# Kernel optimization log

Measured on AMD Instinct MI355X. Metric: run time of the kernel, lower is better.

Reference implementation:

```python
import jax, jax.numpy as jnp
import numpy as np
import math

D_H = 256
H = 4
DK = 64  # d_h // num_heads

def _ff(x, w1, b1, w2, b2):
    # FeedForward: Linear -> GELU -> (dropout, eval=identity) -> Linear -> GELU
    h = jax.nn.gelu(x @ w1 + b1, approximate=False)
    return jax.nn.gelu(h @ w2 + b2, approximate=False)

def _attend(h_t, h_s, tgt, src, nw, num_t, m_w1, m_b1, m_w2, m_b2, Wq, Wk, Wv):
    E = tgt.shape[0]
    M_s = _ff(h_s, m_w1, m_b1, m_w2, m_b2)           # [N_s, d_h]
    Q = h_t @ Wq                                     # [N_t, H*DK]
    K = h_s @ Wk
    V = M_s @ Wv
    Qe = Q[tgt].reshape(E, H, DK)
    Ke = K[src].reshape(E, H, DK)
    Ve = V[src].reshape(E, H, DK)
    scores = (Qe * Ke).sum(-1) / math.sqrt(DK)       # [E, H]
    scores = scores + jnp.log(jnp.clip(nw, 1e-10))[:, None]
    # torch scatter_reduce amax with zeros init + include_self=True => max includes 0
    smax = jnp.maximum(jax.ops.segment_max(scores, tgt, num_segments=num_t), 0.0)
    ex = jnp.exp(scores - smax[tgt])
    sum_ex = jax.ops.segment_sum(ex, tgt, num_segments=num_t)
    attn = ex / (sum_ex[tgt] + 1e-10)                # [E, H]
    wV = (attn[:, :, None] * Ve).reshape(E, H * DK)
    return jax.ops.segment_sum(wV, tgt, num_segments=num_t)  # [N_t, d_h]

def setup_inputs() -> dict:
    key = jax.random.key(0)
    ks = jax.random.split(key, 20)
    I, A, E = 50000, 10000, 200000
    s = 0.05
    return {
        "inv_h": jax.random.normal(ks[0], (I, D_H), jnp.float32),
        "asset_h": jax.random.normal(ks[1], (A, D_H), jnp.float32),
        "inv_norm_w": jax.random.uniform(ks[2], (E,), jnp.float32),
        "asset_norm_w": jax.random.uniform(ks[3], (E,), jnp.float32),
        "m_w1": jax.random.normal(ks[4], (D_H, D_H), jnp.float32) * s,
        "m_b1": jnp.zeros((D_H,), jnp.float32),
        "m_w2": jax.random.normal(ks[5], (D_H, D_H), jnp.float32) * s,
        "m_b2": jnp.zeros((D_H,), jnp.float32),
        "Wq": jax.random.normal(ks[6], (D_H, H * DK), jnp.float32) * s,
        "Wk": jax.random.normal(ks[7], (D_H, H * DK), jnp.float32) * s,
        "Wv": jax.random.normal(ks[8], (D_H, H * DK), jnp.float32) * s,
        "u_w1": jax.random.normal(ks[9], (2 * D_H, D_H), jnp.float32) * s,
        "u_b1": jnp.zeros((D_H,), jnp.float32),
        "u_w2": jax.random.normal(ks[10], (D_H, D_H), jnp.float32) * s,
        "u_b2": jnp.zeros((D_H,), jnp.float32),
        "edge_tgt": jax.random.randint(ks[11], (E,), 0, I),
        "edge_src": jax.random.randint(ks[12], (E,), 0, A),
    }

def reference(inv_h, asset_h, inv_norm_w, asset_norm_w,
              m_w1, m_b1, m_w2, m_b2, Wq, Wk, Wv,
              u_w1, u_b1, u_w2, u_b2, edge_tgt, edge_src):
    I = inv_h.shape[0]
    A = asset_h.shape[0]
    # investors aggregate from assets: edge_index_ia = (inv, asset)
    inv_msg = _attend(inv_h, asset_h, edge_tgt, edge_src, inv_norm_w, I,
                      m_w1, m_b1, m_w2, m_b2, Wq, Wk, Wv)
    # assets aggregate from investors: reversed edges
    asset_msg = _attend(asset_h, inv_h, edge_src, edge_tgt, asset_norm_w, A,
                        m_w1, m_b1, m_w2, m_b2, Wq, Wk, Wv)
    inv_h_new = _ff(jnp.concatenate([inv_h, inv_msg], axis=-1), u_w1, u_b1, u_w2, u_b2)
    asset_h_new = _ff(jnp.concatenate([asset_h, asset_msg], axis=-1), u_w1, u_b1, u_w2, u_b2)
    return (inv_h_new, asset_h_new)
```

## Files before the change

### kernel.cpp

```cpp
#include <hip/hip_runtime.h>

typedef __bf16 bf16x8 __attribute__((ext_vector_type(8)));
typedef float f32x16 __attribute__((ext_vector_type(16)));
typedef unsigned short ushort8 __attribute__((ext_vector_type(8)));

__device__ __forceinline__ float gelu_exact(float x) {
    return 0.5f * x * (1.0f + erff(x * 0.70710678118654752440f));
}

__device__ __forceinline__ void gload_lds16(const void* g, void* l) {
    __builtin_amdgcn_global_load_lds(
        (const __attribute__((address_space(1))) unsigned int*)g,
        (__attribute__((address_space(3))) unsigned int*)l, 16, 0, 0);
}


__global__ __launch_bounds__(256) void count_kernel(
    const int* __restrict__ tgt, const int* __restrict__ src,
    int* __restrict__ cnt_i, int* __restrict__ cnt_a, int E)
{
    int e = blockIdx.x * 256 + threadIdx.x;
    if (e < E) {
        atomicAdd(&cnt_i[tgt[e]], 1);
        atomicAdd(&cnt_a[src[e]], 1);
    }
}

__global__ __launch_bounds__(256) void scan_block(
    const int* __restrict__ cnt, int* __restrict__ offs, int* __restrict__ bsum, int N)
{
    __shared__ int s[256];
    int i = blockIdx.x * 256 + threadIdx.x;
    int v = (i < N) ? cnt[i] : 0;
    s[threadIdx.x] = v;
    __syncthreads();
    for (int d = 1; d < 256; d <<= 1) {
        int t = (threadIdx.x >= d) ? s[threadIdx.x - d] : 0;
        __syncthreads();
        s[threadIdx.x] += t;
        __syncthreads();
    }
    if (i < N) offs[i] = s[threadIdx.x] - v;
    if (threadIdx.x == 255) bsum[blockIdx.x] = s[255];
}

__global__ __launch_bounds__(256) void scan_bsum(int* __restrict__ bsum, int nb)
{
    __shared__ int s[256];
    int v = (threadIdx.x < nb) ? bsum[threadIdx.x] : 0;
    s[threadIdx.x] = v;
    __syncthreads();
    for (int d = 1; d < 256; d <<= 1) {
        int t = (threadIdx.x >= d) ? s[threadIdx.x - d] : 0;
        __syncthreads();
        s[threadIdx.x] += t;
        __syncthreads();
    }
    if (threadIdx.x < nb) bsum[threadIdx.x] = s[threadIdx.x] - v;
}

__global__ __launch_bounds__(256) void add_offs(
    int* __restrict__ offs, int* __restrict__ cursor,
    const int* __restrict__ bsum, int N, int E)
{
    int i = blockIdx.x * 256 + threadIdx.x;
    if (i < N) {
        int f = offs[i] + bsum[blockIdx.x];
        offs[i] = f;
        cursor[i] = f;
    }
    if (i == 0) offs[N] = E;
}

__global__ __launch_bounds__(256) void fill_kernel(
    const int* __restrict__ tgt, const int* __restrict__ src,
    const float* __restrict__ nw_i, const float* __restrict__ nw_a,
    int* __restrict__ cur_i, int* __restrict__ cur_a,
    int* __restrict__ src_i, float* __restrict__ lw_i,
    int* __restrict__ src_a, float* __restrict__ lw_a, int E)
{
    int e = blockIdx.x * 256 + threadIdx.x;
    if (e < E) {
        int t = tgt[e], s = src[e];
        float li = logf(fmaxf(nw_i[e], 1e-10f));
        float la = logf(fmaxf(nw_a[e], 1e-10f));
        int p = atomicAdd(&cur_i[t], 1);
        src_i[p] = s; lw_i[p] = li;
        int q = atomicAdd(&cur_a[s], 1);
        src_a[q] = t; lw_a[q] = la;
    }
}

struct PrepArgs {
    const float* src[7];
    unsigned short* hi[7];
    unsigned short* lo[7];
    int K[7];
    int off[8];
};

__global__ __launch_bounds__(256) void prep_w(PrepArgs a)
{
    int s = blockIdx.x * 256 + threadIdx.x;
    if (s >= a.off[7]) return;
    int m = 0;
    #pragma unroll
    for (int i = 0; i < 6; ++i) m += (s >= a.off[i + 1]) ? 1 : 0;
    int sl = s - a.off[m];
    int KB = a.K[m] >> 4;
    int l  = sl & 63;
    int kb = (sl >> 6) % KB;
    int nb = (sl >> 6) / KB;
    int n  = nb * 32 + (l & 31);
    int k0 = kb * 16 + ((l >> 5) << 3);
    ushort8 hh, ll;
    #pragma unroll
    for (int i = 0; i < 8; ++i) {
        float x = a.src[m][(size_t)(k0 + i) * 256 + n];
        __bf16 h = (__bf16)x;
        hh[i] = __builtin_bit_cast(unsigned short, h);
        ll[i] = __builtin_bit_cast(unsigned short, (__bf16)(x - (float)h));
    }
    *(ushort8*)(a.hi[m] + (size_t)sl * 8) = hh;
    *(ushort8*)(a.lo[m] + (size_t)sl * 8) = ll;
}

__global__ __launch_bounds__(256) void pack_rows(
    const float* __restrict__ X, unsigned short* __restrict__ Ph,
    unsigned short* __restrict__ Pl, int M, int RB)
{
    int s = blockIdx.x * 256 + threadIdx.x;
    int total = RB * 16 * 64;
    if (s >= total) return;
    int l  = s & 63;
    int kb = (s >> 6) & 15;
    int rb = s >> 10;
    int row = min(rb * 32 + (l & 31), M - 1);
    int k0  = kb * 16 + ((l >> 5) << 3);
    const float* p = X + (size_t)row * 256 + k0;
    float4 f0 = *(const float4*)p;
    float4 f1 = *(const float4*)(p + 4);
    float xs[8] = {f0.x, f0.y, f0.z, f0.w, f1.x, f1.y, f1.z, f1.w};
    ushort8 hh, ll;
    #pragma unroll
    for (int i = 0; i < 8; ++i) {
        __bf16 h = (__bf16)xs[i];
        hh[i] = __builtin_bit_cast(unsigned short, h);
        ll[i] = __builtin_bit_cast(unsigned short, (__bf16)(xs[i] - (float)h));
    }
    *(ushort8*)(Ph + (size_t)s * 8) = hh;
    *(ushort8*)(Pl + (size_t)s * 8) = ll;
}

__global__ __launch_bounds__(256) void fused_attn(
    const float* __restrict__ Q, const float* __restrict__ Kk, const float* __restrict__ V,
    const int* __restrict__ offs, const int* __restrict__ srcs,
    const float* __restrict__ lws,
    float* __restrict__ scbuf, unsigned short* __restrict__ msgH,
    unsigned short* __restrict__ msgL, int T)
{
    int w = blockIdx.x * 4 + (threadIdx.x >> 6);
    int lane = threadIdx.x & 63;
    if (w >= T) return;
    int t = w;
    int beg = offs[t], end = offs[t + 1];
    int h = lane >> 4;

    float4 q = *(const float4*)(Q + (size_t)t * 256 + lane * 4);

    float mx = 0.f;
    {
        int sN = 0; float lC = 0.f, lN = 0.f;
        float4 k0 = make_float4(0.f, 0.f, 0.f, 0.f);
        if (beg < end) {
            int s0 = srcs[beg];
            lC = lws[beg];
            k0 = *(const float4*)(Kk + (size_t)s0 * 256 + lane * 4);
        }
        if (beg + 1 < end) { sN = srcs[beg + 1]; lN = lws[beg + 1]; }
        for (int j = beg; j < end; ++j) {
            int sNN = 0; float lNN = 0.f;
            if (j + 2 < end) { sNN = srcs[j + 2]; lNN = lws[j + 2]; }
            float4 k1 = k0;
            if (j + 1 < end) k1 = *(const float4*)(Kk + (size_t)sN * 256 + lane * 4);
            float d = q.x * k0.x + q.y * k0.y + q.z * k0.z + q.w * k0.w;
            d += __shfl_xor(d, 1);
            d += __shfl_xor(d, 2);
            d += __shfl_xor(d, 4);
            d += __shfl_xor(d, 8);
            float sc = d * 0.125f + lC;
            if ((lane & 15) == 0) scbuf[(size_t)j * 4 + h] = sc;
            mx = fmaxf(mx, sc);
            k0 = k1; lC = lN; sN = sNN; lN = lNN;
        }
    }

    float sum = 0.f;
    float4 macc = make_float4(0.f, 0.f, 0.f, 0.f);
    {
        int sN = 0; float scC = 0.f, scN = 0.f;
        float4 v0 = make_float4(0.f, 0.f, 0.f, 0.f);
        if (beg < end) {
            int s0 = srcs[beg];
            scC = scbuf[(size_t)beg * 4 + h];
            v0 = *(const float4*)(V + (size_t)s0 * 256 + lane * 4);
        }
        if (beg + 1 < end) { sN = srcs[beg + 1]; scN = scbuf[(size_t)(beg + 1) * 4 + h]; }
        for (int j = beg; j < end; ++j) {
            int sNN = 0; float scNN = 0.f;
            if (j + 2 < end) { sNN = srcs[j + 2]; scNN = scbuf[(size_t)(j + 2) * 4 + h]; }
            float4 v1 = v0;
            if (j + 1 < end) v1 = *(const float4*)(V + (size_t)sN * 256 + lane * 4);
            float ex = expf(scC - mx);
            sum += ex;
            macc.x += ex * v0.x; macc.y += ex * v0.y;
            macc.z += ex * v0.z; macc.w += ex * v0.w;
            v0 = v1; scC = scN; sN = sNN; scN = scNN;
        }
    }
    float inv = 1.f / (sum + 1e-10f);
    float vals[4] = {macc.x * inv, macc.y * inv, macc.z * inv, macc.w * inv};
    unsigned short hs[4], ls[4];
    #pragma unroll
    for (int i = 0; i < 4; ++i) {
        __bf16 hh = (__bf16)vals[i];
        hs[i] = __builtin_bit_cast(unsigned short, hh);
        ls[i] = __builtin_bit_cast(unsigned short, (__bf16)(vals[i] - (float)hh));
    }
    size_t base = (((size_t)(t >> 5) * 16 + (lane >> 2)) * 64 + ((lane >> 1) & 1) * 32 + (t & 31)) * 8
                + ((lane & 1) << 2);
    *(ushort4*)(msgH + base) = make_ushort4(hs[0], hs[1], hs[2], hs[3]);
    *(ushort4*)(msgL + base) = make_ushort4(ls[0], ls[1], ls[2], ls[3]);
}

template<int CONCAT, int PACKOUT>
__global__ __launch_bounds__(256, 2) void gemm_pk(
    const unsigned short* __restrict__ Ah, const unsigned short* __restrict__ Al,
    const unsigned short* __restrict__ A2h, const unsigned short* __restrict__ A2l,
    const unsigned short* __restrict__ Bh, const unsigned short* __restrict__ Bl,
    const float* __restrict__ bias, int act, int M,
    float* __restrict__ Cf, unsigned short* __restrict__ Ch, unsigned short* __restrict__ Cl)
{
    const int KB = CONCAT ? 32 : 16;
    const int NS = CONCAT ? 8 : 4;
    const int RB = (M + 31) >> 5;
    const int lane = threadIdx.x & 63;
    const int w = threadIdx.x >> 6;
    const int rbb = blockIdx.x * 2;
    const int nb0 = w * 2;

    __shared__ union {
        unsigned short stage[3][2][2][4][512];
        float tbuf[4][32 * 33];
    } sm __attribute__((aligned(16)));

    f32x16 acc[2][2] = {};

    auto stage_one = [&](int bufn, int st, int u) {
        int half = u >> 3, rb = (u >> 2) & 1, kb = u & 3;
        int kbg = st * 4 + kb;
        const unsigned short* srcp;
        int kba = kbg;
        if (CONCAT && kbg >= 16) { kba = kbg - 16; srcp = half ? A2l : A2h; }
        else                     { srcp = half ? Al : Ah; }
        int rbl = min(rbb + rb, RB - 1);
        const unsigned short* g = srcp + ((size_t)(rbl * 16 + kba) * 64 + lane) * 8;
        gload_lds16(g, &sm.stage[bufn][half][rb][kb][0]);
    };

    #pragma unroll
    for (int i = 0; i < 4; ++i) stage_one(0, 0, w * 4 + i);
    #pragma unroll
    for (int i = 0; i < 4; ++i) stage_one(1, 1, w * 4 + i);
    asm volatile("s_waitcnt vmcnt(4)" ::: "memory");
    __builtin_amdgcn_s_barrier();

    for (int st = 0; st < NS; ++st) {
        if (st) {
            asm volatile("s_waitcnt vmcnt(20)" ::: "memory");
            __builtin_amdgcn_s_barrier();
        }
        const int buf = st % 3;

        ushort8 Breg[4][4];
        #pragma unroll
        for (int kb = 0; kb < 4; ++kb) {
            int kbg = st * 4 + kb;
            size_t t0 = ((size_t)((nb0 + 0) * KB + kbg) * 64 + lane) * 8;
            size_t t1 = ((size_t)((nb0 + 1) * KB + kbg) * 64 + lane) * 8;
            Breg[kb][0] = *(const ushort8*)(Bh + t0);
            Breg[kb][1] = *(const ushort8*)(Bl + t0);
            Breg[kb][2] = *(const ushort8*)(Bh + t1);
            Breg[kb][3] = *(const ushort8*)(Bl + t1);
        }

        {
            int bufn = (st + 2) % 3;
            int stc = (st + 2 < NS) ? (st + 2) : (NS - 1);
            #pragma unroll
            for (int i = 0; i < 4; ++i) stage_one(bufn, stc, w * 4 + i);
        }

        #pragma unroll
        for (int kb = 0; kb < 4; ++kb) {
            bf16x8 a0h = __builtin_bit_cast(bf16x8, *(const ushort8*)&sm.stage[buf][0][0][kb][lane * 8]);
            bf16x8 a0l = __builtin_bit_cast(bf16x8, *(const ushort8*)&sm.stage[buf][1][0][kb][lane * 8]);
            bf16x8 a1h = __builtin_bit_cast(bf16x8, *(const ushort8*)&sm.stage[buf][0][1][kb][lane * 8]);
            bf16x8 a1l = __builtin_bit_cast(bf16x8, *(const ushort8*)&sm.stage[buf][1][1][kb][lane * 8]);
            bf16x8 b0h = __builtin_bit_cast(bf16x8, Breg[kb][0]);
            bf16x8 b0l = __builtin_bit_cast(bf16x8, Breg[kb][1]);
            bf16x8 b1h = __builtin_bit_cast(bf16x8, Breg[kb][2]);
            bf16x8 b1l = __builtin_bit_cast(bf16x8, Breg[kb][3]);
            acc[0][0] = __builtin_amdgcn_mfma_f32_32x32x16_bf16(a0h, b0h, acc[0][0], 0, 0, 0);
            acc[0][0] = __builtin_amdgcn_mfma_f32_32x32x16_bf16(a0h, b0l, acc[0][0], 0, 0, 0);
            acc[0][0] = __builtin_amdgcn_mfma_f32_32x32x16_bf16(a0l, b0h, acc[0][0], 0, 0, 0);
            acc[0][1] = __builtin_amdgcn_mfma_f32_32x32x16_bf16(a0h, b1h, acc[0][1], 0, 0, 0);
            acc[0][1] = __builtin_amdgcn_mfma_f32_32x32x16_bf16(a0h, b1l, acc[0][1], 0, 0, 0);
            acc[0][1] = __builtin_amdgcn_mfma_f32_32x32x16_bf16(a0l, b1h, acc[0][1], 0, 0, 0);
            acc[1][0] = __builtin_amdgcn_mfma_f32_32x32x16_bf16(a1h, b0h, acc[1][0], 0, 0, 0);
            acc[1][0] = __builtin_amdgcn_mfma_f32_32x32x16_bf16(a1h, b0l, acc[1][0], 0, 0, 0);
            acc[1][0] = __builtin_amdgcn_mfma_f32_32x32x16_bf16(a1l, b0h, acc[1][0], 0, 0, 0);
            acc[1][1] = __builtin_amdgcn_mfma_f32_32x32x16_bf16(a1h, b1h, acc[1][1], 0, 0, 0);
            acc[1][1] = __builtin_amdgcn_mfma_f32_32x32x16_bf16(a1h, b1l, acc[1][1], 0, 0, 0);
            acc[1][1] = __builtin_amdgcn_mfma_f32_32x32x16_bf16(a1l, b1h, acc[1][1], 0, 0, 0);
        }
    }

    asm volatile("s_waitcnt vmcnt(0)" ::: "memory");
    __builtin_amdgcn_s_barrier();

    const int m2 = lane & 31;
    #pragma unroll
    for (int mt = 0; mt < 2; ++mt) {
        int rb = rbb + mt;
        bool rvalid = rb < RB;
        int mg = rb * 32 + m2;
        #pragma unroll
        for (int nt = 0; nt < 2; ++nt) {
            int nb = nb0 + nt;
            float bv = bias ? bias[nb * 32 + (lane & 31)] : 0.f;
            #pragma unroll
            for (int r = 0; r < 16; ++r) {
                int ml = (r & 3) + ((r >> 2) << 3) + ((lane >> 5) << 2);
                float v = acc[mt][nt][r] + bv;
                if (act) v = gelu_exact(v);
                sm.tbuf[w][ml * 33 + (lane & 31)] = v;
            }
            asm volatile("s_waitcnt lgkmcnt(0)" ::: "memory");
            #pragma unroll
            for (int qq = 0; qq < 2; ++qq) {
                int c0 = ((lane >> 5) << 3) + (qq << 4);
                float vs[8];
                #pragma unroll
                for (int i = 0; i < 8; ++i) vs[i] = sm.tbuf[w][m2 * 33 + c0 + i];
                if (PACKOUT) {
                    ushort8 hh, ll;
                    #pragma unroll
                    for (int i = 0; i < 8; ++i) {
                        __bf16 hb = (__bf16)vs[i];
                        hh[i] = __builtin_bit_cast(unsigned short, hb);
                        ll[i] = __builtin_bit_cast(unsigned short, (__bf16)(vs[i] - (float)hb));
                    }
                    int ng = nb * 32 + c0;
                    size_t slot = (((size_t)rb * 16 + (ng >> 4)) * 64 + ((ng >> 3) & 1) * 32 + m2) * 8;
                    if (rvalid) {
                        *(ushort8*)(Ch + slot) = hh;
                        *(ushort8*)(Cl + slot) = ll;
                    }
                } else {
                    if (mg < M) {
                        float* cp = Cf + (size_t)mg * 256 + nb * 32 + c0;
                        *(float4*)(cp)     = make_float4(vs[0], vs[1], vs[2], vs[3]);
                        *(float4*)(cp + 4) = make_float4(vs[4], vs[5], vs[6], vs[7]);
                    }
                }
            }
            asm volatile("s_waitcnt lgkmcnt(0)" ::: "memory");
        }
    }
}

extern "C" void kernel_launch(void* const* d_in, const int* in_sizes, int n_in,
                              void* d_out, int out_size, void* d_ws, size_t ws_size,
                              hipStream_t stream) {
    const float* inv_h    = (const float*)d_in[0];
    const float* asset_h  = (const float*)d_in[1];
    const float* inv_nw   = (const float*)d_in[2];
    const float* asset_nw = (const float*)d_in[3];
    const float* m_w1 = (const float*)d_in[4];
    const float* m_b1 = (const float*)d_in[5];
    const float* m_w2 = (const float*)d_in[6];
    const float* m_b2 = (const float*)d_in[7];
    const float* Wq   = (const float*)d_in[8];
    const float* Wk   = (const float*)d_in[9];
    const float* Wv   = (const float*)d_in[10];
    const float* u_w1 = (const float*)d_in[11];
    const float* u_b1 = (const float*)d_in[12];
    const float* u_w2 = (const float*)d_in[13];
    const float* u_b2 = (const float*)d_in[14];
    const int* etgt  = (const int*)d_in[15];
    const int* esrc  = (const int*)d_in[16];

    const int I = in_sizes[0] / 256;
    const int A = in_sizes[1] / 256;
    const int E = in_sizes[15];
    const int RBI = (I + 31) >> 5;
    const int RBA = (A + 31) >> 5;

    float* out_inv   = (float*)d_out;
    float* out_asset = (float*)d_out + (size_t)I * 256;

    char* wsp = (char*)d_ws;
    size_t off = 0;
    auto alloc = [&](size_t bytes) -> char* {
        char* p = wsp + off;
        off += (bytes + 255) & ~(size_t)255;
        return p;
    };

    const size_t ipackHalf = (size_t)RBI * 16384;
    const size_t apackHalf = (size_t)RBA * 16384;
    const size_t if32 = (size_t)I * 1024;
    const size_t af32 = (size_t)A * 1024;
    const size_t r_sz = (2 * ipackHalf > if32) ? 2 * ipackHalf : if32;
    const size_t s_sz = (2 * apackHalf > af32) ? 2 * apackHalf : af32;

    unsigned short* invP_h  = (unsigned short*)alloc(ipackHalf);
    unsigned short* invP_l  = (unsigned short*)alloc(ipackHalf);
    unsigned short* astP_h  = (unsigned short*)alloc(apackHalf);
    unsigned short* astP_l  = (unsigned short*)alloc(apackHalf);
    char* R1 = alloc(r_sz);
    char* R2 = alloc(r_sz);
    char* S1 = alloc(s_sz);
    char* S2 = alloc(s_sz);
    char* S3 = alloc(s_sz);
    float* scbuf = (float*)alloc((size_t)E * 4 * 4);
    int* cnt_i  = (int*)alloc((size_t)I * 4);
    int* cnt_a  = (int*)alloc((size_t)A * 4);
    int* offs_i = (int*)alloc((size_t)(I + 1) * 4);
    int* offs_a = (int*)alloc((size_t)(A + 1) * 4);
    int* gsrc_i = (int*)alloc((size_t)E * 4);
    int* gsrc_a = (int*)alloc((size_t)E * 4);
    float* glw_i = (float*)alloc((size_t)E * 4);
    float* glw_a = (float*)alloc((size_t)E * 4);
    int* bsum_i = (int*)alloc(256 * 4);
    int* bsum_a = (int*)alloc(256 * 4);

    PrepArgs pa;
    const float* wsrc[7] = {m_w1, m_w2, Wq, Wk, Wv, u_w1, u_w2};
    const int    wK[7]   = {256, 256, 256, 256, 256, 512, 256};
    unsigned short* wph[7];
    unsigned short* wpl[7];
    pa.off[0] = 0;
    for (int i = 0; i < 7; ++i) {
        size_t slots = (size_t)(wK[i] >> 4) * 8 * 64;
        wph[i] = (unsigned short*)alloc(slots * 16);
        wpl[i] = (unsigned short*)alloc(slots * 16);
        pa.src[i] = wsrc[i];
        pa.hi[i] = wph[i];
        pa.lo[i] = wpl[i];
        pa.K[i] = wK[i];
        pa.off[i + 1] = pa.off[i] + (int)slots;
    }

    const int nbI = (I + 255) / 256;
    const int nbA = (A + 255) / 256;
    const int nbE = (E + 255) / 256;

    hipLaunchKernelGGL(prep_w, dim3((pa.off[7] + 255) / 256), dim3(256), 0, stream, pa);
    hipLaunchKernelGGL(pack_rows, dim3((RBI * 1024 + 255) / 256), dim3(256), 0, stream,
                       inv_h, invP_h, invP_l, I, RBI);
    hipLaunchKernelGGL(pack_rows, dim3((RBA * 1024 + 255) / 256), dim3(256), 0, stream,
                       asset_h, astP_h, astP_l, A, RBA);

    hipMemsetAsync(cnt_i, 0, (size_t)I * 4, stream);
    hipMemsetAsync(cnt_a, 0, (size_t)A * 4, stream);
    hipLaunchKernelGGL(count_kernel, dim3(nbE), dim3(256), 0, stream,
                       etgt, esrc, cnt_i, cnt_a, E);
    hipLaunchKernelGGL(scan_block, dim3(nbI), dim3(256), 0, stream, cnt_i, offs_i, bsum_i, I);
    hipLaunchKernelGGL(scan_block, dim3(nbA), dim3(256), 0, stream, cnt_a, offs_a, bsum_a, A);
    hipLaunchKernelGGL(scan_bsum, dim3(1), dim3(256), 0, stream, bsum_i, nbI);
    hipLaunchKernelGGL(scan_bsum, dim3(1), dim3(256), 0, stream, bsum_a, nbA);
    hipLaunchKernelGGL(add_offs, dim3(nbI), dim3(256), 0, stream, offs_i, cnt_i, bsum_i, I, E);
    hipLaunchKernelGGL(add_offs, dim3(nbA), dim3(256), 0, stream, offs_a, cnt_a, bsum_a, A, E);
    hipLaunchKernelGGL(fill_kernel, dim3(nbE), dim3(256), 0, stream,
                       etgt, esrc, inv_nw, asset_nw, cnt_i, cnt_a,
                       gsrc_i, glw_i, gsrc_a, glw_a, E);

    auto gemm = [&](const unsigned short* aH, const unsigned short* aL,
                    const unsigned short* a2H, const unsigned short* a2L,
                    int M, int widx, const float* bias, int act,
                    float* cf, unsigned short* cH, unsigned short* cL, int concat) {
        dim3 grid((((M + 31) >> 5) + 1) / 2);
        if (concat) {
            if (cf) hipLaunchKernelGGL((gemm_pk<1,0>), grid, dim3(256), 0, stream,
                        aH, aL, a2H, a2L, wph[widx], wpl[widx], bias, act, M, cf, cH, cL);
            else    hipLaunchKernelGGL((gemm_pk<1,1>), grid, dim3(256), 0, stream,
                        aH, aL, a2H, a2L, wph[widx], wpl[widx], bias, act, M, cf, cH, cL);
        } else {
            if (cf) hipLaunchKernelGGL((gemm_pk<0,0>), grid, dim3(256), 0, stream,
                        aH, aL, a2H, a2L, wph[widx], wpl[widx], bias, act, M, cf, cH, cL);
            else    hipLaunchKernelGGL((gemm_pk<0,1>), grid, dim3(256), 0, stream,
                        aH, aL, a2H, a2L, wph[widx], wpl[widx], bias, act, M, cf, cH, cL);
        }
    };

    auto ph = [&](char* r) { return (unsigned short*)r; };
    auto plI = [&](char* r) { return (unsigned short*)(r + ipackHalf); };
    auto plA = [&](char* r) { return (unsigned short*)(r + apackHalf); };

    gemm(invP_h, invP_l, 0, 0, I, 0, m_b1, 1, nullptr, ph(R1), plI(R1), 0);
    gemm(ph(R1), plI(R1), 0, 0, I, 1, m_b2, 1, nullptr, ph(R2), plI(R2), 0);
    gemm(ph(R2), plI(R2), 0, 0, I, 4, nullptr, 0, (float*)R1, 0, 0, 0);
    gemm(invP_h, invP_l, 0, 0, I, 3, nullptr, 0, (float*)R2, 0, 0, 0);
    gemm(astP_h, astP_l, 0, 0, A, 2, nullptr, 0, (float*)S1, 0, 0, 0);

    hipLaunchKernelGGL(fused_attn, dim3((A + 3) / 4), dim3(256), 0, stream,
                       (float*)S1, (float*)R2, (float*)R1, offs_a, gsrc_a, glw_a,
                       scbuf, ph(S2), plA(S2), A);

    gemm(astP_h, astP_l, ph(S2), plA(S2), A, 5, u_b1, 1, nullptr, ph(S3), plA(S3), 1);
    gemm(ph(S3), plA(S3), 0, 0, A, 6, u_b2, 1, out_asset, 0, 0, 0);

    gemm(astP_h, astP_l, 0, 0, A, 0, m_b1, 1, nullptr, ph(S1), plA(S1), 0);
    gemm(ph(S1), plA(S1), 0, 0, A, 1, m_b2, 1, nullptr, ph(S2), plA(S2), 0);
    gemm(ph(S2), plA(S2), 0, 0, A, 4, nullptr, 0, (float*)S1, 0, 0, 0);
    gemm(astP_h, astP_l, 0, 0, A, 3, nullptr, 0, (float*)S2, 0, 0, 0);
    gemm(invP_h, invP_l, 0, 0, I, 2, nullptr, 0, (float*)R1, 0, 0, 0);

    hipLaunchKernelGGL(fused_attn, dim3((I + 3) / 4), dim3(256), 0, stream,
                       (float*)R1, (float*)S2, (float*)S1, offs_i, gsrc_i, glw_i,
                       scbuf, ph(R2), plI(R2), I);

    gemm(invP_h, invP_l, ph(R2), plI(R2), I, 5, u_b1, 1, nullptr, ph(R1), plI(R1), 1);
    gemm(ph(R1), plI(R1), 0, 0, I, 6, u_b2, 1, out_inv, 0, 0, 0);
}
```

Measured before the change: 835.9 us.

## Fuse per-node GEMM chains into single kernels keeping intermediates in LDS

Replaces the sequence of separate packed-bf16 GEMM launches with two fused kernels. One computes K, Q, and the message FFN plus V projection per 32-row block, with the A tile staged once in LDS and the intermediate GELU outputs repacked into LDS. The other does the concat update FFN, with its hidden layer kept in LDS. This removes intermediate global round-trips and about 14 launches, and computes both node types' projections up front. In exchange, each block handles 32 rows instead of 64, B operands are read straight from global inside the fused GEMMs without prefetch, and outputs use scalar strided stores instead of transposed vector stores.

```diff
diff --git a/kernel.cpp b/kernel.cpp
--- a/kernel.cpp
+++ b/kernel.cpp
@@ -13,6 +13,8 @@
         (const __attribute__((address_space(1))) unsigned int*)g,
         (__attribute__((address_space(3))) unsigned int*)l, 16, 0, 0);
 }
+
+#define MFMA(a, b, c) __builtin_amdgcn_mfma_f32_32x32x16_bf16((a), (b), (c), 0, 0, 0)
 
 
 __global__ __launch_bounds__(256) void count_kernel(
@@ -233,150 +235,168 @@
     *(ushort4*)(msgL + base) = make_ushort4(ls[0], ls[1], ls[2], ls[3]);
 }
 
-template<int CONCAT, int PACKOUT>
-__global__ __launch_bounds__(256, 2) void gemm_pk(
+template<int MODE>
+__global__ __launch_bounds__(256, 3) void fused_node(
     const unsigned short* __restrict__ Ah, const unsigned short* __restrict__ Al,
     const unsigned short* __restrict__ A2h, const unsigned short* __restrict__ A2l,
-    const unsigned short* __restrict__ Bh, const unsigned short* __restrict__ Bl,
-    const float* __restrict__ bias, int act, int M,
-    float* __restrict__ Cf, unsigned short* __restrict__ Ch, unsigned short* __restrict__ Cl)
-{
-    const int KB = CONCAT ? 32 : 16;
-    const int NS = CONCAT ? 8 : 4;
-    const int RB = (M + 31) >> 5;
+    const unsigned short* __restrict__ B1h, const unsigned short* __restrict__ B1l,
+    const unsigned short* __restrict__ B2h, const unsigned short* __restrict__ B2l,
+    const unsigned short* __restrict__ B3h, const unsigned short* __restrict__ B3l,
+    const unsigned short* __restrict__ B4h, const unsigned short* __restrict__ B4l,
+    const unsigned short* __restrict__ B5h, const unsigned short* __restrict__ B5l,
+    const float* __restrict__ bias1, const float* __restrict__ bias2,
+    int M,
+    float* __restrict__ O1, float* __restrict__ O2, float* __restrict__ O3)
+{
+    extern __shared__ char smem[];
+    unsigned short* sus = (unsigned short*)smem;
     const int lane = threadIdx.x & 63;
     const int w = threadIdx.x >> 6;
-    const int rbb = blockIdx.x * 2;
     const int nb0 = w * 2;
-
-    __shared__ union {
-        unsigned short stage[3][2][2][4][512];
-        float tbuf[4][32 * 33];
-    } sm __attribute__((aligned(16)));
-
-    f32x16 acc[2][2] = {};
-
-    auto stage_one = [&](int bufn, int st, int u) {
-        int half = u >> 3, rb = (u >> 2) & 1, kb = u & 3;
-        int kbg = st * 4 + kb;
-        const unsigned short* srcp;
-        int kba = kbg;
-        if (CONCAT && kbg >= 16) { kba = kbg - 16; srcp = half ? A2l : A2h; }
-        else                     { srcp = half ? Al : Ah; }
-        int rbl = min(rbb + rb, RB - 1);
-        const unsigned short* g = srcp + ((size_t)(rbl * 16 + kba) * 64 + lane) * 8;
-        gload_lds16(g, &sm.stage[bufn][half][rb][kb][0]);
+    const int rb = blockIdx.x;
+
+    auto gemm_lds = [&](const unsigned short* BH, const unsigned short* BL, int KBw,
+                        f32x16& A0, f32x16& A1) {
+        #pragma unroll 4
+        for (int kb = 0; kb < 16; ++kb) {
+            bf16x8 ah  = __builtin_bit_cast(bf16x8, *(const ushort8*)(smem + kb * 1024 + lane * 16));
+            bf16x8 alo = __builtin_bit_cast(bf16x8, *(const ushort8*)(smem + 16384 + kb * 1024 + lane * 16));
+            size_t t0 = ((size_t)((nb0 + 0) * KBw + kb) * 64 + lane) * 8;
+            size_t t1 = ((size_t)((nb0 + 1) * KBw + kb) * 64 + lane) * 8;
+            bf16x8 b0h = __builtin_bit_cast(bf16x8, *(const ushort8*)(BH + t0));
+            bf16x8 b0l = __builtin_bit_cast(bf16x8, *(const ushort8*)(BL + t0));
+            bf16x8 c1h = __builtin_bit_cast(bf16x8, *(const ushort8*)(BH + t1));
+            bf16x8 c1l = __builtin_bit_cast(bf16x8, *(const ushort8*)(BL + t1));
+            A0 = MFMA(ah, b0h, A0); A0 = MFMA(ah, b0l, A0); A0 = MFMA(alo, b0h, A0);
+            A1 = MFMA(ah, c1h, A1); A1 = MFMA(ah, c1l, A1); A1 = MFMA(alo, c1h, A1);
+        }
     };
 
-    #pragma unroll
-    for (int i = 0; i < 4; ++i) stage_one(0, 0, w * 4 + i);
-    #pragma unroll
-    for (int i = 0; i < 4; ++i) stage_one(1, 1, w * 4 + i);
-    asm volatile("s_waitcnt vmcnt(4)" ::: "memory");
-    __builtin_amdgcn_s_barrier();
-
-    for (int st = 0; st < NS; ++st) {
-        if (st) {
-            asm volatile("s_waitcnt vmcnt(20)" ::: "memory");
-            __builtin_amdgcn_s_barrier();
-        }
-        const int buf = st % 3;
-
-        ushort8 Breg[4][4];
-        #pragma unroll
-        for (int kb = 0; kb < 4; ++kb) {
-            int kbg = st * 4 + kb;
-            size_t t0 = ((size_t)((nb0 + 0) * KB + kbg) * 64 + lane) * 8;
-            size_t t1 = ((size_t)((nb0 + 1) * KB + kbg) * 64 + lane) * 8;
-            Breg[kb][0] = *(const ushort8*)(Bh + t0);
-            Breg[kb][1] = *(const ushort8*)(Bl + t0);
-            Breg[kb][2] = *(const ushort8*)(Bh + t1);
-            Breg[kb][3] = *(const ushort8*)(Bl + t1);
-        }
-
-        {
-            int bufn = (st + 2) % 3;
-            int stc = (st + 2 < NS) ? (st + 2) : (NS - 1);
-            #pragma unroll
-            for (int i = 0; i < 4; ++i) stage_one(bufn, stc, w * 4 + i);
-        }
-
-        #pragma unroll
-        for (int kb = 0; kb < 4; ++kb) {
-            bf16x8 a0h = __builtin_bit_cast(bf16x8, *(const ushort8*)&sm.stage[buf][0][0][kb][lane * 8]);
-            bf16x8 a0l = __builtin_bit_cast(bf16x8, *(const ushort8*)&sm.stage[buf][1][0][kb][lane * 8]);
-            bf16x8 a1h = __builtin_bit_cast(bf16x8, *(const ushort8*)&sm.stage[buf][0][1][kb][lane * 8]);
-            bf16x8 a1l = __builtin_bit_cast(bf16x8, *(const ushort8*)&sm.stage[buf][1][1][kb][lane * 8]);
-            bf16x8 b0h = __builtin_bit_cast(bf16x8, Breg[kb][0]);
-            bf16x8 b0l = __builtin_bit_cast(bf16x8, Breg[kb][1]);
-            bf16x8 b1h = __builtin_bit_cast(bf16x8, Breg[kb][2]);
-            bf16x8 b1l = __builtin_bit_cast(bf16x8, Breg[kb][3]);
-            acc[0][0] = __builtin_amdgcn_mfma_f32_32x32x16_bf16(a0h, b0h, acc[0][0], 0, 0, 0);
-            acc[0][0] = __builtin_amdgcn_mfma_f32_32x32x16_bf16(a0h, b0l, acc[0][0], 0, 0, 0);
-            acc[0][0] = __builtin_amdgcn_mfma_f32_32x32x16_bf16(a0l, b0h, acc[0][0], 0, 0, 0);
-            acc[0][1] = __builtin_amdgcn_mfma_f32_32x32x16_bf16(a0h, b1h, acc[0][1], 0, 0, 0);
-            acc[0][1] = __builtin_amdgcn_mfma_f32_32x32x16_bf16(a0h, b1l, acc[0][1], 0, 0, 0);
-            acc[0][1] = __builtin_amdgcn_mfma_f32_32x32x16_bf16(a0l, b1h, acc[0][1], 0, 0, 0);
-            acc[1][0] = __builtin_amdgcn_mfma_f32_32x32x16_bf16(a1h, b0h, acc[1][0], 0, 0, 0);
-            acc[1][0] = __builtin_amdgcn_mfma_f32_32x32x16_bf16(a1h, b0l, acc[1][0], 0, 0, 0);
-            acc[1][0] = __builtin_amdgcn_mfma_f32_32x32x16_bf16(a1l, b0h, acc[1][0], 0, 0, 0);
-            acc[1][1] = __builtin_amdgcn_mfma_f32_32x32x16_bf16(a1h, b1h, acc[1][1], 0, 0, 0);
-            acc[1][1] = __builtin_amdgcn_mfma_f32_32x32x16_bf16(a1h, b1l, acc[1][1], 0, 0, 0);
-            acc[1][1] = __builtin_amdgcn_mfma_f32_32x32x16_bf16(a1l, b1h, acc[1][1], 0, 0, 0);
-        }
-    }
-
-    asm volatile("s_waitcnt vmcnt(0)" ::: "memory");
-    __builtin_amdgcn_s_barrier();
-
-    const int m2 = lane & 31;
-    #pragma unroll
-    for (int mt = 0; mt < 2; ++mt) {
-        int rb = rbb + mt;
-        bool rvalid = rb < RB;
-        int mg = rb * 32 + m2;
+    auto store_f32 = [&](const f32x16& A0, const f32x16& A1, const float* bias, int act,
+                         float* Out) {
         #pragma unroll
         for (int nt = 0; nt < 2; ++nt) {
-            int nb = nb0 + nt;
-            float bv = bias ? bias[nb * 32 + (lane & 31)] : 0.f;
+            const f32x16& a = nt ? A1 : A0;
+            int n = (nb0 + nt) * 32 + (lane & 31);
+            float bv = bias ? bias[n] : 0.f;
             #pragma unroll
             for (int r = 0; r < 16; ++r) {
-                int ml = (r & 3) + ((r >> 2) << 3) + ((lane >> 5) << 2);
-                float v = acc[mt][nt][r] + bv;
-                if (act) v = gelu_exact(v);
-                sm.tbuf[w][ml * 33 + (lane & 31)] = v;
-            }
-            asm volatile("s_waitcnt lgkmcnt(0)" ::: "memory");
-            #pragma unroll
-            for (int qq = 0; qq < 2; ++qq) {
-                int c0 = ((lane >> 5) << 3) + (qq << 4);
-                float vs[8];
-                #pragma unroll
-                for (int i = 0; i < 8; ++i) vs[i] = sm.tbuf[w][m2 * 33 + c0 + i];
-                if (PACKOUT) {
-                    ushort8 hh, ll;
-                    #pragma unroll
-                    for (int i = 0; i < 8; ++i) {
-                        __bf16 hb = (__bf16)vs[i];
-                        hh[i] = __builtin_bit_cast(unsigned short, hb);
-                        ll[i] = __builtin_bit_cast(unsigned short, (__bf16)(vs[i] - (float)hb));
-                    }
-                    int ng = nb * 32 + c0;
-                    size_t slot = (((size_t)rb * 16 + (ng >> 4)) * 64 + ((ng >> 3) & 1) * 32 + m2) * 8;
-                    if (rvalid) {
-                        *(ushort8*)(Ch + slot) = hh;
-                        *(ushort8*)(Cl + slot) = ll;
-                    }
-                } else {
-                    if (mg < M) {
-                        float* cp = Cf + (size_t)mg * 256 + nb * 32 + c0;
-                        *(float4*)(cp)     = make_float4(vs[0], vs[1], vs[2], vs[3]);
-                        *(float4*)(cp + 4) = make_float4(vs[4], vs[5], vs[6], vs[7]);
-                    }
+                int row = rb * 32 + (r & 3) + ((r >> 2) << 3) + ((lane >> 5) << 2);
+                if (row < M) {
+                    float v = a[r] + bv;
+                    if (act) v = gelu_exact(v);
+                    Out[(size_t)row * 256 + n] = v;
                 }
             }
-            asm volatile("s_waitcnt lgkmcnt(0)" ::: "memory");
-        }
+        }
+    };
+
+    auto pack_to_lds = [&](const f32x16& A0, const f32x16& A1, const float* bias) {
+        #pragma unroll
+        for (int nt = 0; nt < 2; ++nt) {
+            const f32x16& a = nt ? A1 : A0;
+            int n = (nb0 + nt) * 32 + (lane & 31);
+            float bv = bias[n];
+            int ub = (n >> 4) * 512 + ((n >> 3) & 1) * 256 + (n & 7);
+            #pragma unroll
+            for (int r = 0; r < 16; ++r) {
+                int m = (r & 3) + ((r >> 2) << 3) + ((lane >> 5) << 2);
+                float v = gelu_exact(a[r] + bv);
+                __bf16 hb = (__bf16)v;
+                sus[ub + m * 8] = __builtin_bit_cast(unsigned short, hb);
+                sus[8192 + ub + m * 8] =
+                    __builtin_bit_cast(unsigned short, (__bf16)(v - (float)hb));
+            }
+        }
+    };
+
+    if constexpr (MODE == 0) {
+        #pragma unroll
+        for (int i = 0; i < 8; ++i) {
+            int u = w * 8 + i, hl = u >> 4, kb = u & 15;
+            const unsigned short* srcp = hl ? Al : Ah;
+            const unsigned short* g = srcp + ((size_t)(rb * 16 + kb) * 64 + lane) * 8;
+            gload_lds16(g, smem + hl * 16384 + kb * 1024);
+        }
+        asm volatile("s_waitcnt vmcnt(0)" ::: "memory");
+        __builtin_amdgcn_s_barrier();
+
+        { f32x16 a0 = {}, a1 = {}; gemm_lds(B1h, B1l, 16, a0, a1);
+          store_f32(a0, a1, nullptr, 0, O1); }
+        { f32x16 a0 = {}, a1 = {}; gemm_lds(B2h, B2l, 16, a0, a1);
+          store_f32(a0, a1, nullptr, 0, O2); }
+        f32x16 t0 = {}, t1 = {};
+        gemm_lds(B3h, B3l, 16, t0, t1);
+        __syncthreads();
+        pack_to_lds(t0, t1, bias1);
+        __syncthreads();
+        f32x16 m0 = {}, m1 = {};
+        gemm_lds(B4h, B4l, 16, m0, m1);
+        __syncthreads();
+        pack_to_lds(m0, m1, bias2);
+        __syncthreads();
+        { f32x16 a0 = {}, a1 = {}; gemm_lds(B5h, B5l, 16, a0, a1);
+          store_f32(a0, a1, nullptr, 0, O3); }
+    } else {
+        auto stage_one = [&](int bufn, int st, int u) {
+            int hl = u >> 2, kb = u & 3;
+            int kbg = st * 4 + kb;
+            const unsigned short* srcp; int kba = kbg;
+            if (kbg >= 16) { kba = kbg - 16; srcp = hl ? A2l : A2h; }
+            else           { srcp = hl ? Al : Ah; }
+            const unsigned short* g = srcp + ((size_t)(rb * 16 + kba) * 64 + lane) * 8;
+            gload_lds16(g, smem + bufn * 8192 + (hl * 4 + kb) * 1024);
+        };
+        stage_one(0, 0, w * 2); stage_one(0, 0, w * 2 + 1);
+        stage_one(1, 1, w * 2); stage_one(1, 1, w * 2 + 1);
+        asm volatile("s_waitcnt vmcnt(2)" ::: "memory");
+        __builtin_amdgcn_s_barrier();
+
+        f32x16 h0 = {}, h1 = {};
+        for (int st = 0; st < 8; ++st) {
+            if (st) {
+                asm volatile("s_waitcnt vmcnt(18)" ::: "memory");
+                __builtin_amdgcn_s_barrier();
+            }
+            const int buf = st % 3;
+            ushort8 Breg[4][4];
+            #pragma unroll
+            for (int kb = 0; kb < 4; ++kb) {
+                int kbg = st * 4 + kb;
+                size_t t0 = ((size_t)((nb0 + 0) * 32 + kbg) * 64 + lane) * 8;
+                size_t t1 = ((size_t)((nb0 + 1) * 32 + kbg) * 64 + lane) * 8;
+                Breg[kb][0] = *(const ushort8*)(B1h + t0);
+                Breg[kb][1] = *(const ushort8*)(B1l + t0);
+                Breg[kb][2] = *(const ushort8*)(B1h + t1);
+                Breg[kb][3] = *(const ushort8*)(B1l + t1);
+            }
+            {
+                int bufn = (st + 2) % 3;
+                int stc = (st + 2 < 8) ? (st + 2) : 7;
+                stage_one(bufn, stc, w * 2);
+                stage_one(bufn, stc, w * 2 + 1);
+            }
+            #pragma unroll
+            for (int kb = 0; kb < 4; ++kb) {
+                bf16x8 ah  = __builtin_bit_cast(bf16x8,
+                    *(const ushort8*)(smem + buf * 8192 + kb * 1024 + lane * 16));
+                bf16x8 alo = __builtin_bit_cast(bf16x8,
+                    *(const ushort8*)(smem + buf * 8192 + (4 + kb) * 1024 + lane * 16));
+                bf16x8 b0h = __builtin_bit_cast(bf16x8, Breg[kb][0]);
+                bf16x8 b0l = __builtin_bit_cast(bf16x8, Breg[kb][1]);
+                bf16x8 c1h = __builtin_bit_cast(bf16x8, Breg[kb][2]);
+                bf16x8 c1l = __builtin_bit_cast(bf16x8, Breg[kb][3]);
+                h0 = MFMA(ah, b0h, h0); h0 = MFMA(ah, b0l, h0); h0 = MFMA(alo, b0h, h0);
+                h1 = MFMA(ah, c1h, h1); h1 = MFMA(ah, c1l, h1); h1 = MFMA(alo, c1h, h1);
+            }
+        }
+        asm volatile("s_waitcnt vmcnt(0)" ::: "memory");
+        __builtin_amdgcn_s_barrier();
+
+        pack_to_lds(h0, h1, bias1);
+        __syncthreads();
+        { f32x16 o0 = {}, o1 = {}; gemm_lds(B2h, B2l, 16, o0, o1);
+          store_f32(o0, o1, bias2, 1, O3); }
     }
 }
 
@@ -420,20 +440,22 @@
 
     const size_t ipackHalf = (size_t)RBI * 16384;
     const size_t apackHalf = (size_t)RBA * 16384;
-    const size_t if32 = (size_t)I * 1024;
-    const size_t af32 = (size_t)A * 1024;
-    const size_t r_sz = (2 * ipackHalf > if32) ? 2 * ipackHalf : if32;
-    const size_t s_sz = (2 * apackHalf > af32) ? 2 * apackHalf : af32;
-
-    unsigned short* invP_h  = (unsigned short*)alloc(ipackHalf);
-    unsigned short* invP_l  = (unsigned short*)alloc(ipackHalf);
-    unsigned short* astP_h  = (unsigned short*)alloc(apackHalf);
-    unsigned short* astP_l  = (unsigned short*)alloc(apackHalf);
-    char* R1 = alloc(r_sz);
-    char* R2 = alloc(r_sz);
-    char* S1 = alloc(s_sz);
-    char* S2 = alloc(s_sz);
-    char* S3 = alloc(s_sz);
+
+    unsigned short* invP_h = (unsigned short*)alloc(ipackHalf);
+    unsigned short* invP_l = (unsigned short*)alloc(ipackHalf);
+    unsigned short* astP_h = (unsigned short*)alloc(apackHalf);
+    unsigned short* astP_l = (unsigned short*)alloc(apackHalf);
+    char* KfI_raw = alloc(2 * ipackHalf);
+    float* KfI = (float*)KfI_raw;
+    unsigned short* msgI_h = (unsigned short*)KfI_raw;
+    unsigned short* msgI_l = (unsigned short*)(KfI_raw + ipackHalf);
+    float* QfI = (float*)alloc((size_t)I * 1024);
+    float* VfI = (float*)alloc((size_t)I * 1024);
+    float* KfA = (float*)alloc((size_t)A * 1024);
+    float* QfA = (float*)alloc((size_t)A * 1024);
+    float* VfA = (float*)alloc((size_t)A * 1024);
+    unsigned short* msgA_h = (unsigned short*)alloc(apackHalf);
+    unsigned short* msgA_l = (unsigned short*)alloc(apackHalf);
     float* scbuf = (float*)alloc((size_t)E * 4 * 4);
     int* cnt_i  = (int*)alloc((size_t)I * 4);
     int* cnt_a  = (int*)alloc((size_t)A * 4);
@@ -487,51 +509,38 @@
                        etgt, esrc, inv_nw, asset_nw, cnt_i, cnt_a,
                        gsrc_i, glw_i, gsrc_a, glw_a, E);
 
-    auto gemm = [&](const unsigned short* aH, const unsigned short* aL,
-                    const unsigned short* a2H, const unsigned short* a2L,
-                    int M, int widx, const float* bias, int act,
-                    float* cf, unsigned short* cH, unsigned short* cL, int concat) {
-        dim3 grid((((M + 31) >> 5) + 1) / 2);
-        if (concat) {
-            if (cf) hipLaunchKernelGGL((gemm_pk<1,0>), grid, dim3(256), 0, stream,
-                        aH, aL, a2H, a2L, wph[widx], wpl[widx], bias, act, M, cf, cH, cL);
-            else    hipLaunchKernelGGL((gemm_pk<1,1>), grid, dim3(256), 0, stream,
-                        aH, aL, a2H, a2L, wph[widx], wpl[widx], bias, act, M, cf, cH, cL);
-        } else {
-            if (cf) hipLaunchKernelGGL((gemm_pk<0,0>), grid, dim3(256), 0, stream,
-                        aH, aL, a2H, a2L, wph[widx], wpl[widx], bias, act, M, cf, cH, cL);
-            else    hipLaunchKernelGGL((gemm_pk<0,1>), grid, dim3(256), 0, stream,
-                        aH, aL, a2H, a2L, wph[widx], wpl[widx], bias, act, M, cf, cH, cL);
-        }
-    };
-
-    auto ph = [&](char* r) { return (unsigned short*)r; };
-    auto plI = [&](char* r) { return (unsigned short*)(r + ipackHalf); };
-    auto plA = [&](char* r) { return (unsigned short*)(r + apackHalf); };
-
-    gemm(invP_h, invP_l, 0, 0, I, 0, m_b1, 1, nullptr, ph(R1), plI(R1), 0);
-    gemm(ph(R1), plI(R1), 0, 0, I, 1, m_b2, 1, nullptr, ph(R2), plI(R2), 0);
-    gemm(ph(R2), plI(R2), 0, 0, I, 4, nullptr, 0, (float*)R1, 0, 0, 0);
-    gemm(invP_h, invP_l, 0, 0, I, 3, nullptr, 0, (float*)R2, 0, 0, 0);
-    gemm(astP_h, astP_l, 0, 0, A, 2, nullptr, 0, (float*)S1, 0, 0, 0);
+    hipLaunchKernelGGL((fused_node<0>), dim3(RBI), dim3(256), 32768, stream,
+                       invP_h, invP_l, (const unsigned short*)nullptr, (const unsigned short*)nullptr,
+                       wph[3], wpl[3],
+                       wph[2], wpl[2],
+                       wph[0], wpl[0],
+                       wph[1], wpl[1],
+                       wph[4], wpl[4],
+                       m_b1, m_b2, I, KfI, QfI, VfI);
+    hipLaunchKernelGGL((fused_node<0>), dim3(RBA), dim3(256), 32768, stream,
+                       astP_h, astP_l, (const unsigned short*)nullptr, (const unsigned short*)nullptr,
+                       wph[3], wpl[3], wph[2], wpl[2], wph[0], wpl[0],
+                       wph[1], wpl[1], wph[4], wpl[4],
+                       m_b1, m_b2, A, KfA, QfA, VfA);
 
     hipLaunchKernelGGL(fused_attn, dim3((A + 3) / 4), dim3(256), 0, stream,
-                       (float*)S1, (float*)R2, (float*)R1, offs_a, gsrc_a, glw_a,
-                       scbuf, ph(S2), plA(S2), A);
-
-    gemm(astP_h, astP_l, ph(S2), plA(S2), A, 5, u_b1, 1, nullptr, ph(S3), plA(S3), 1);
-    gemm(ph(S3), plA(S3), 0, 0, A, 6, u_b2, 1, out_asset, 0, 0, 0);
-
-    gemm(astP_h, astP_l, 0, 0, A, 0, m_b1, 1, nullptr, ph(S1), plA(S1), 0);
-    gemm(ph(S1), plA(S1), 0, 0, A, 1, m_b2, 1, nullptr, ph(S2), plA(S2), 0);
-    gemm(ph(S2), plA(S2), 0, 0, A, 4, nullptr, 0, (float*)S1, 0, 0, 0);
-    gemm(astP_h, astP_l, 0, 0, A, 3, nullptr, 0, (float*)S2, 0, 0, 0);
-    gemm(invP_h, invP_l, 0, 0, I, 2, nullptr, 0, (float*)R1, 0, 0, 0);
-
+                       QfA, KfI, VfI, offs_a, gsrc_a, glw_a, scbuf, msgA_h, msgA_l, A);
     hipLaunchKernelGGL(fused_attn, dim3((I + 3) / 4), dim3(256), 0, stream,
-                       (float*)R1, (float*)S2, (float*)S1, offs_i, gsrc_i, glw_i,
-                       scbuf, ph(R2), plI(R2), I);
-
-    gemm(invP_h, invP_l, ph(R2), plI(R2), I, 5, u_b1, 1, nullptr, ph(R1), plI(R1), 1);
-    gemm(ph(R1), plI(R1), 0, 0, I, 6, u_b2, 1, out_inv, 0, 0, 0);
-}
+                       QfI, KfA, VfA, offs_i, gsrc_i, glw_i, scbuf, msgI_h, msgI_l, I);
+
+    hipLaunchKernelGGL((fused_node<1>), dim3(RBA), dim3(256), 32768, stream,
+                       astP_h, astP_l, msgA_h, msgA_l,
+                       wph[5], wpl[5],
+                       wph[6], wpl[6],
+                       (const unsigned short*)nullptr, (const unsigned short*)nullptr,
+                       (const unsigned short*)nullptr, (const unsigned short*)nullptr,
+                       (const unsigned short*)nullptr, (const unsigned short*)nullptr,
+                       u_b1, u_b2, A, (float*)nullptr, (float*)nullptr, out_asset);
+    hipLaunchKernelGGL((fused_node<1>), dim3(RBI), dim3(256), 32768, stream,
+                       invP_h, invP_l, msgI_h, msgI_l,
+                       wph[5], wpl[5], wph[6], wpl[6],
+                       (const unsigned short*)nullptr, (const unsigned short*)nullptr,
+                       (const unsigned short*)nullptr, (const unsigned short*)nullptr,
+                       (const unsigned short*)nullptr, (const unsigned short*)nullptr,
+                       u_b1, u_b2, I, (float*)nullptr, (float*)nullptr, out_inv);
+}
```

After: 701.0 us. 1.19x faster.
